# Performance work log

Hardware: AMD Instinct MI355X
Metric: run time of the kernel (lower is better)

## Reference

```python
import jax, jax.numpy as jnp
import numpy as np

EPS = 1e-6
N, CHANNEL, M, K, D = 4096, 1024, 8, 2048, 128


def setup_inputs() -> dict:
    key = jax.random.key(0)
    ks = jax.random.split(key, 7)
    std = float(np.sqrt(2.0 / (5.0 * CHANNEL / M)))  # matches nn.init.normal_ std in __init__
    return {
        "x": jax.random.normal(ks[0], (N, CHANNEL), dtype=jnp.float32),
        "codebook0": jax.random.normal(ks[1], (M, K, D), dtype=jnp.float32) * std,
        "codebook1": jax.random.normal(ks[2], (M, K, D), dtype=jnp.float32) * std,
        "temperature0": jnp.ones((M, 1), dtype=jnp.float32),
        "temperature1": jnp.ones((M, 1), dtype=jnp.float32),
        "u0": jax.random.uniform(ks[3], (N, M, K), dtype=jnp.float32),
        "u1": jax.random.uniform(ks[4], (N, M, K), dtype=jnp.float32),
    }


def _distance(z, codebook):
    # z: (n, m, d), codebook: (m, k, d) -> (n, m, k) squared euclidean
    x2 = jnp.sum(z * z, axis=-1, keepdims=True)          # (n, m, 1)
    c2 = jnp.sum(codebook * codebook, axis=-1)           # (m, k)
    inter = jnp.einsum('nmd,mkd->nmk', z, codebook)      # (n, m, k)
    return x2 + c2 - 2.0 * inter


def _level(x, codebook, temperature, u):
    # One _quantizerEncoder level with Identity heads.
    n = x.shape[0]
    m, k, d = codebook.shape
    z = x.reshape(n, m, d)
    scale = jnp.asarray(np.sqrt(k), dtype=x.dtype)
    # logit = -distance / sqrt(k) * LowerBound(temperature, Eps)
    logit = (-_distance(z, codebook) / scale) * jnp.maximum(temperature, EPS)
    # gumbel-softmax, tau=1.0, hard=True (permutationRate == 0 -> no permutation)
    uc = jnp.clip(u, EPS, 1.0 - EPS)
    gumbel = -jnp.log(-jnp.log(uc))
    y = jax.nn.softmax(logit + gumbel, axis=-1)          # (n, m, k)
    hard_idx = jnp.argmax(y, axis=-1)                    # (n, m)
    y_hard = jax.nn.one_hot(hard_idx, k, dtype=y.dtype)
    sample = y_hard + y - jax.lax.stop_gradient(y)       # straight-through
    # _multiCodebookDeQuantization.forward
    deq = jnp.einsum('nmk,mkd->nmd', sample, codebook).reshape(n, m * d)
    return sample, deq, logit


def reference(x, codebook0, codebook1, temperature0, temperature1, u0, u1):
    # Encoder pass (Identity latentStageEncoder/quantizationHead/latentHead)
    _, deq0, _ = _level(x, codebook0, temperature0, u0)
    x1 = x - deq0                                        # residual to next level
    _, deq1, _ = _level(x1, codebook1, temperature1, u1)
    # Decoder pass, reversed (Identity dequantizationHead/sideHead/restoreHead):
    # formerLevel = decode(level1); xHat = deq0 + sideHead(formerLevel)
    former = deq1
    xHat = deq0 + former
    return xHat
```

## Files before the change

kernel.cpp:

```cpp
#include <hip/hip_runtime.h>
#include <math.h>


namespace {
constexpr int Mm = 8, Kk = 2048, Dd = 128;
constexpr int MK = Mm * Kk;
constexpr double SQRTK = 45.254833995939045;
constexpr double MARGIN = 0.05;

__device__ __forceinline__ double wsum_d(double v) {
#pragma unroll
  for (int o = 32; o > 0; o >>= 1) v += __shfl_xor(v, o);
  return v;
}
__device__ __forceinline__ float wsum_f(float v) {
#pragma unroll
  for (int o = 32; o > 0; o >>= 1) v += __shfl_xor(v, o);
  return v;
}
__device__ __forceinline__ float wmax_f(float v) {
#pragma unroll
  for (int o = 32; o > 0; o >>= 1) v = fmaxf(v, __shfl_xor(v, o));
  return v;
}

__device__ __forceinline__ double gumbel_d(float u) {
  double uc = fmin(fmax((double)u, 1e-6), 1.0 - 1e-6);
  return -log(-log(uc));
}

__global__ __launch_bounds__(256) void prep1(
    const float* __restrict__ cb0, const float* __restrict__ cb1,
    double* __restrict__ c2d0, double* __restrict__ c2d1) {
  int wid = threadIdx.x >> 6, lane = threadIdx.x & 63;
  int row = blockIdx.x * 4 + wid;
  int lvl = row >= MK;
  int r = row & (MK - 1);
  const float* cb = lvl ? cb1 : cb0;
  float2 c = ((const float2*)(cb + (size_t)r * Dd))[lane];
  double s = wsum_d((double)c.x * (double)c.x + (double)c.y * (double)c.y);
  if (lane == 0) { if (lvl) c2d1[r] = s; else c2d0[r] = s; }
}

__global__ __launch_bounds__(256) void prep2(
    const double* __restrict__ c2d0, const double* __restrict__ c2d1,
    const float* __restrict__ t0, const float* __restrict__ t1,
    float2* __restrict__ Rtab) {
  int b = blockIdx.x;
  int lvl = b >> 3, m = b & 7;
  const double* c2 = (lvl ? c2d1 : c2d0) + m * Kk;
  int tid = threadIdx.x;
  double mx = -1e300, mn = 1e300;
  for (int i = tid; i < Kk; i += 256) { double v = c2[i]; mx = fmax(mx, v); mn = fmin(mn, v); }
#pragma unroll
  for (int o = 32; o > 0; o >>= 1) {
    mx = fmax(mx, __shfl_xor(mx, o));
    mn = fmin(mn, __shfl_xor(mn, o));
  }
  __shared__ double smx[4], smn[4];
  int wid = tid >> 6, lane = tid & 63;
  if (lane == 0) { smx[wid] = mx; smn[wid] = mn; }
  __syncthreads();
  if (tid == 0) {
    mx = fmax(fmax(smx[0], smx[1]), fmax(smx[2], smx[3]));
    mn = fmin(fmin(smn[0], smn[1]), fmin(smn[2], smn[3]));
    double w = (double)fmaxf(lvl ? t1[m] : t0[m], 1e-6f) / SQRTK;
    float2 r;
    r.x = (float)(w * (mx - mn) * 1.0001);
    r.y = (float)(4.0 * w * sqrt(mx) * 1.0001);
    Rtab[b] = r;
  }
}

__device__ __forceinline__ int do_level(
    float zx, float zy, int lane,
    const float* __restrict__ urow,
    const float* __restrict__ cbm,
    const double* __restrict__ c2m,
    float2 rr, double wd) {
  const float4* u4 = (const float4*)urow;
  float4 r[8];
  float um = 0.f;
#pragma unroll
  for (int j = 0; j < 8; ++j) {
    r[j] = u4[j * 64 + lane];
    um = fmaxf(um, fmaxf(fmaxf(r[j].x, r[j].y), fmaxf(r[j].z, r[j].w)));
  }
  um = wmax_f(um);
  float zn = sqrtf(wsum_f(zx * zx + zy * zy));
  double thr = gumbel_d(um) - (double)(rr.x + rr.y * zn) - MARGIN;
  float uthr = (float)(exp(-exp(-thr)) * (1.0 - 1e-7));
  unsigned mask32 = 0;
#pragma unroll
  for (int j = 0; j < 8; ++j) {
    mask32 |= (r[j].x >= uthr ? 1u : 0u) << (j * 4 + 0);
    mask32 |= (r[j].y >= uthr ? 1u : 0u) << (j * 4 + 1);
    mask32 |= (r[j].z >= uthr ? 1u : 0u) << (j * 4 + 2);
    mask32 |= (r[j].w >= uthr ? 1u : 0u) << (j * 4 + 3);
  }
  double bestS = -1e300;
  int bestK = 0;
  while (true) {
    unsigned long long wm = __ballot(mask32 != 0);
    if (!wm) break;
    int l = (int)__ffsll(wm) - 1;
    unsigned lm = (unsigned)__shfl((int)mask32, l);
    int t = __builtin_ffs((int)lm) - 1;
    if (lane == l) mask32 &= mask32 - 1;
    int kc = ((t >> 2) << 8) + (l << 2) + (t & 3);
    float2 c = ((const float2*)(cbm + (size_t)kc * Dd))[lane];
    double dot = wsum_d((double)zx * (double)c.x + (double)zy * (double)c.y);
    double sc = (2.0 * dot - c2m[kc]) * wd + gumbel_d(urow[kc]);
    if (sc > bestS || (sc == bestS && kc < bestK)) { bestS = sc; bestK = kc; }
  }
  return bestK;
}

__global__ __launch_bounds__(256) void fused_kernel(
    const float* __restrict__ x,
    const float* __restrict__ cb0, const float* __restrict__ cb1,
    const float* __restrict__ t0, const float* __restrict__ t1,
    const float* __restrict__ u0, const float* __restrict__ u1,
    const double* __restrict__ c2d0, const double* __restrict__ c2d1,
    const float2* __restrict__ Rtab,
    float* __restrict__ out) {
  const int wid = threadIdx.x >> 6, lane = threadIdx.x & 63;
  const int p = blockIdx.x * 4 + wid;
  const int m = p >> 12;
  const int n = p & 4095;

  float2 z = ((const float2*)(x + (size_t)n * 1024 + m * Dd))[lane];
  double wd0 = (double)fmaxf(t0[m], 1e-6f) / SQRTK;
  double wd1 = (double)fmaxf(t1[m], 1e-6f) / SQRTK;

  const float* u0row = u0 + ((size_t)n * Mm + m) * Kk;
  const float* u1row = u1 + ((size_t)n * Mm + m) * Kk;
  const float* cb0m = cb0 + (size_t)m * Kk * Dd;
  const float* cb1m = cb1 + (size_t)m * Kk * Dd;

  int b0 = do_level(z.x, z.y, lane, u0row, cb0m, c2d0 + m * Kk, Rtab[m], wd0);
  float2 c0 = ((const float2*)(cb0m + (size_t)b0 * Dd))[lane];

  int b1 = do_level(z.x - c0.x, z.y - c0.y, lane, u1row, cb1m, c2d1 + m * Kk,
                    Rtab[8 + m], wd1);
  float2 c1 = ((const float2*)(cb1m + (size_t)b1 * Dd))[lane];

  ((float2*)(out + (size_t)n * 1024 + m * Dd))[lane] =
      make_float2(c0.x + c1.x, c0.y + c1.y);
}
}

extern "C" void kernel_launch(void* const* d_in, const int* in_sizes, int n_in,
                              void* d_out, int out_size, void* d_ws, size_t ws_size,
                              hipStream_t stream) {
  const float* x   = (const float*)d_in[0];
  const float* cb0 = (const float*)d_in[1];
  const float* cb1 = (const float*)d_in[2];
  const float* t0  = (const float*)d_in[3];
  const float* t1  = (const float*)d_in[4];
  const float* u0  = (const float*)d_in[5];
  const float* u1  = (const float*)d_in[6];
  float* out = (float*)d_out;

  char* ws = (char*)d_ws;
  double* c2d0 = (double*)ws;
  double* c2d1 = c2d0 + MK;
  float2* Rtab = (float2*)(c2d1 + MK);

  prep1<<<8192, 256, 0, stream>>>(cb0, cb1, c2d0, c2d1);
  prep2<<<16, 256, 0, stream>>>(c2d0, c2d1, t0, t1, Rtab);
  fused_kernel<<<8192, 256, 0, stream>>>(x, cb0, cb1, t0, t1, u0, u1,
                                         c2d0, c2d1, Rtab, out);
}
```

Measured before the change: 572.2 us.

## Prefetch both levels' noise rows, batch candidate gumbels, use fast float threshold

Both u0 and u1 rows are now loaded up front so the second level's noise fetch overlaps the first level's work. Candidate processing is restructured so each lane computes its own candidate's gumbel term in parallel before the wave iterates over the batch, instead of doing one serial scalar load and double log per candidate. The pruning threshold is computed in float with fast intrinsics and a conservative lower-bound gumbel approximation. The winning codebook vector is kept in registers so the final reload is skipped. The float threshold path relies on its widened safety margins to stay exact, which is a correctness risk if those margins are too tight.

```diff
diff --git a/kernel.cpp b/kernel.cpp
--- a/kernel.cpp
+++ b/kernel.cpp
@@ -6,7 +6,6 @@
 constexpr int Mm = 8, Kk = 2048, Dd = 128;
 constexpr int MK = Mm * Kk;
 constexpr double SQRTK = 45.254833995939045;
-constexpr double MARGIN = 0.05;
 
 __device__ __forceinline__ double wsum_d(double v) {
 #pragma unroll
@@ -27,6 +26,19 @@
 __device__ __forceinline__ double gumbel_d(float u) {
   double uc = fmin(fmax((double)u, 1e-6), 1.0 - 1e-6);
   return -log(-log(uc));
+}
+
+__device__ __forceinline__ float gumbel_lb_f(float u) {
+  float uc = fminf(fmaxf(u, 1e-6f), 1.0f - 1e-6f);
+  float e = 1.0f - uc;
+  float t;
+  if (e > 0.04f) {
+    t = -__logf(uc);
+  } else {
+    t = e * (1.0f + e * (0.5f + e * (0.3333334f + e * 0.25f)));
+  }
+  t *= 1.000004f;
+  return -__logf(t) - 2e-5f;
 }
 
 __global__ __launch_bounds__(256) void prep1(
@@ -73,23 +85,14 @@
 }
 
 __device__ __forceinline__ int do_level(
-    float zx, float zy, int lane,
+    float zx, float zy, int lane, float um, const float4* r,
     const float* __restrict__ urow,
     const float* __restrict__ cbm,
     const double* __restrict__ c2m,
-    float2 rr, double wd) {
-  const float4* u4 = (const float4*)urow;
-  float4 r[8];
-  float um = 0.f;
-#pragma unroll
-  for (int j = 0; j < 8; ++j) {
-    r[j] = u4[j * 64 + lane];
-    um = fmaxf(um, fmaxf(fmaxf(r[j].x, r[j].y), fmaxf(r[j].z, r[j].w)));
-  }
-  um = wmax_f(um);
+    float2 rr, double wd, float2* bc_out) {
   float zn = sqrtf(wsum_f(zx * zx + zy * zy));
-  double thr = gumbel_d(um) - (double)(rr.x + rr.y * zn) - MARGIN;
-  float uthr = (float)(exp(-exp(-thr)) * (1.0 - 1e-7));
+  float thr = gumbel_lb_f(um) - (rr.x + rr.y * zn) - 0.05f;
+  float uthr = __expf(-__expf(-thr) * 1.000004f) * (1.0f - 4e-6f);
   unsigned mask32 = 0;
 #pragma unroll
   for (int j = 0; j < 8; ++j) {
@@ -100,19 +103,33 @@
   }
   double bestS = -1e300;
   int bestK = 0;
-  while (true) {
-    unsigned long long wm = __ballot(mask32 != 0);
-    if (!wm) break;
-    int l = (int)__ffsll(wm) - 1;
-    unsigned lm = (unsigned)__shfl((int)mask32, l);
-    int t = __builtin_ffs((int)lm) - 1;
-    if (lane == l) mask32 &= mask32 - 1;
-    int kc = ((t >> 2) << 8) + (l << 2) + (t & 3);
-    float2 c = ((const float2*)(cbm + (size_t)kc * Dd))[lane];
-    double dot = wsum_d((double)zx * (double)c.x + (double)zy * (double)c.y);
-    double sc = (2.0 * dot - c2m[kc]) * wd + gumbel_d(urow[kc]);
-    if (sc > bestS || (sc == bestS && kc < bestK)) { bestS = sc; bestK = kc; }
-  }
+  float2 bc = make_float2(0.f, 0.f);
+  for (;;) {
+    bool has = (mask32 != 0);
+    unsigned long long actv = __ballot(has);
+    if (!actv) break;
+    int kc = 0;
+    double g = 0.0;
+    if (has) {
+      int t = __builtin_ffs((int)mask32) - 1;
+      mask32 &= mask32 - 1;
+      kc = ((t >> 2) << 8) + (lane << 2) + (t & 3);
+      g = gumbel_d(urow[kc]);
+    }
+    while (actv) {
+      int l = (int)__ffsll(actv) - 1;
+      actv &= actv - 1;
+      int kcl = __shfl(kc, l);
+      double gl = __shfl(g, l);
+      float2 c = ((const float2*)(cbm + (size_t)kcl * Dd))[lane];
+      double dot = wsum_d((double)zx * (double)c.x + (double)zy * (double)c.y);
+      double sc = (2.0 * dot - c2m[kcl]) * wd + gl;
+      if (sc > bestS || (sc == bestS && kcl < bestK)) {
+        bestS = sc; bestK = kcl; bc = c;
+      }
+    }
+  }
+  *bc_out = bc;
   return bestK;
 }
 
@@ -129,21 +146,36 @@
   const int m = p >> 12;
   const int n = p & 4095;
 
+  const float* u0row = u0 + ((size_t)n * Mm + m) * Kk;
+  const float* u1row = u1 + ((size_t)n * Mm + m) * Kk;
+  const float4* a4 = (const float4*)u0row;
+  const float4* b4 = (const float4*)u1row;
+
+  float4 r0[8], r1[8];
+#pragma unroll
+  for (int j = 0; j < 8; ++j) { r0[j] = a4[j * 64 + lane]; r1[j] = b4[j * 64 + lane]; }
+
   float2 z = ((const float2*)(x + (size_t)n * 1024 + m * Dd))[lane];
   double wd0 = (double)fmaxf(t0[m], 1e-6f) / SQRTK;
   double wd1 = (double)fmaxf(t1[m], 1e-6f) / SQRTK;
 
-  const float* u0row = u0 + ((size_t)n * Mm + m) * Kk;
-  const float* u1row = u1 + ((size_t)n * Mm + m) * Kk;
+  float um0 = 0.f, um1 = 0.f;
+#pragma unroll
+  for (int j = 0; j < 8; ++j) {
+    um0 = fmaxf(um0, fmaxf(fmaxf(r0[j].x, r0[j].y), fmaxf(r0[j].z, r0[j].w)));
+    um1 = fmaxf(um1, fmaxf(fmaxf(r1[j].x, r1[j].y), fmaxf(r1[j].z, r1[j].w)));
+  }
+  um0 = wmax_f(um0);
+  um1 = wmax_f(um1);
+
   const float* cb0m = cb0 + (size_t)m * Kk * Dd;
   const float* cb1m = cb1 + (size_t)m * Kk * Dd;
 
-  int b0 = do_level(z.x, z.y, lane, u0row, cb0m, c2d0 + m * Kk, Rtab[m], wd0);
-  float2 c0 = ((const float2*)(cb0m + (size_t)b0 * Dd))[lane];
-
-  int b1 = do_level(z.x - c0.x, z.y - c0.y, lane, u1row, cb1m, c2d1 + m * Kk,
-                    Rtab[8 + m], wd1);
-  float2 c1 = ((const float2*)(cb1m + (size_t)b1 * Dd))[lane];
+  float2 c0, c1;
+  (void)do_level(z.x, z.y, lane, um0, r0, u0row, cb0m, c2d0 + m * Kk,
+                 Rtab[m], wd0, &c0);
+  (void)do_level(z.x - c0.x, z.y - c0.y, lane, um1, r1, u1row, cb1m,
+                 c2d1 + m * Kk, Rtab[8 + m], wd1, &c1);
 
   ((float2*)(out + (size_t)n * 1024 + m * Dd))[lane] =
       make_float2(c0.x + c1.x, c0.y + c1.y);
```

Result: no change. 562.6 us (-1.7%).
